# Kernel optimization log

Hardware: AMD Instinct MI355X
Metric: run time of the kernel (lower is better)

## Reference

```python
import jax, jax.numpy as jnp
import numpy as np

N = 100000      # nodes
E = 3200000     # edges
F_IN = 256      # in_channels
H = 64          # hidden_channels
C = 2           # out_channels
G = 128         # graphs in batch


def setup_inputs() -> dict:
    key = jax.random.key(0)
    ks = jax.random.split(key, 10)
    x = jax.random.normal(ks[0], (N, F_IN), jnp.float32)
    edge_index = jax.random.randint(ks[1], (2, E), 0, N, dtype=jnp.int64)
    batch = jnp.sort(jax.random.randint(ks[2], (N,), 0, G, dtype=jnp.int64))
    s = 0.05
    W1 = jax.random.normal(ks[3], (F_IN, H), jnp.float32) * s
    b1 = jnp.zeros((H,), jnp.float32)
    W2 = jax.random.normal(ks[4], (H, H), jnp.float32) * s
    b2 = jnp.zeros((H,), jnp.float32)
    fc_W = jax.random.normal(ks[5], (H, C), jnp.float32) * s
    fc_b = jnp.zeros((C,), jnp.float32)
    return {"x": x, "edge_index": edge_index, "batch": batch,
            "W1": W1, "b1": b1, "W2": W2, "b2": b2,
            "fc_W": fc_W, "fc_b": fc_b}


def _gcn_layer(h, src, dst, norm, W, b, n_nodes):
    # PyG GCNConv: linear transform first, then normalized aggregate, then bias
    h = h @ W                                   # [N, H]
    msg = h[src] * norm[:, None]                # [E+N, H] gather + scale
    out = jax.ops.segment_sum(msg, dst, num_segments=n_nodes)
    return out + b


def reference(x, edge_index, batch, W1, b1, W2, b2, fc_W, fc_b):
    n_nodes = x.shape[0]
    # add self loops (GCNConv default)
    loop = jnp.arange(n_nodes, dtype=edge_index.dtype)
    src = jnp.concatenate([edge_index[0], loop])
    dst = jnp.concatenate([edge_index[1], loop])
    # symmetric normalization D^{-1/2} (A+I) D^{-1/2}
    deg = jax.ops.segment_sum(jnp.ones_like(src, dtype=x.dtype), dst,
                              num_segments=n_nodes)
    deg_isqrt = jnp.where(deg > 0, jax.lax.rsqrt(deg), 0.0)
    norm = deg_isqrt[src] * deg_isqrt[dst]

    h = jax.nn.relu(_gcn_layer(x, src, dst, norm, W1, b1, n_nodes))
    h = jax.nn.relu(_gcn_layer(h, src, dst, norm, W2, b2, n_nodes))

    # global mean pool over graphs
    n_graphs = G
    sums = jax.ops.segment_sum(h, batch, num_segments=n_graphs)
    cnts = jax.ops.segment_sum(jnp.ones((n_nodes,), h.dtype), batch,
                               num_segments=n_graphs)
    pooled = sums / jnp.clip(cnts, 1.0)[:, None]  # [G, H]
    return pooled @ fc_W + fc_b                   # [G, C]
```

## Files before the change

### kernel.cpp

```cpp
#include <hip/hip_runtime.h>
#include <hip/hip_bf16.h>


#define F_IN 256
#define HDIM 64
#define BR_SHIFT 7
#define BRANGE 128
#define BCAP 4608
#define CHUNK 8192
#define NBK 788
#define HS_SCALE 32.0f

typedef short short8 __attribute__((ext_vector_type(8)));
typedef short short4v __attribute__((ext_vector_type(4)));
typedef float float4v __attribute__((ext_vector_type(4)));

__device__ __forceinline__ unsigned bf16_rn(float f) {
  unsigned u = __builtin_bit_cast(unsigned, f);
  return (u + 0x7FFFu + ((u >> 16) & 1u)) >> 16;
}
__device__ __forceinline__ float bf16_to_f32(unsigned h) {
  return __builtin_bit_cast(float, h << 16);
}
__device__ __forceinline__ unsigned char f32_to_fp8(float v) {
  unsigned r = (unsigned)__builtin_amdgcn_cvt_pk_fp8_f32(v, v, 0, false);
  return (unsigned char)(r & 0xFF);
}
__device__ __forceinline__ float4v fp8x4_to_f32x4(unsigned u) {
  float4v r;
  r[0] = __builtin_amdgcn_cvt_f32_fp8(u, 0);
  r[1] = __builtin_amdgcn_cvt_f32_fp8(u, 1);
  r[2] = __builtin_amdgcn_cvt_f32_fp8(u, 2);
  r[3] = __builtin_amdgcn_cvt_f32_fp8(u, 3);
  return r;
}

__global__ __launch_bounds__(256) void bin_kernel(
    const int* __restrict__ src, const int* __restrict__ dst,
    int* __restrict__ gcur, int* __restrict__ entries, int E, int nb) {
  __shared__ int out32[CHUNK];
  __shared__ int pref[NBK + 1];
  __shared__ int cur[NBK];
  __shared__ int gbase[NBK];
  __shared__ int sscan[256];
  const int tid = threadIdx.x;
  for (int i = tid; i < nb; i += 256) cur[i] = 0;
  __syncthreads();
  long e0 = (long)blockIdx.x * CHUNK;
  int cnt = (int)min((long)CHUNK, (long)E - e0);
  for (int i = tid; i < cnt; i += 256)
    atomicAdd(&cur[dst[e0 + i] >> BR_SHIFT], 1);
  __syncthreads();
  int b0 = tid * 4;
  int h[4];
  int s = 0;
#pragma unroll
  for (int i = 0; i < 4; ++i) {
    h[i] = (b0 + i < nb) ? cur[b0 + i] : 0;
    s += h[i];
  }
  int x = s;
  sscan[tid] = x;
  __syncthreads();
  for (int off = 1; off < 256; off <<= 1) {
    int t = (tid >= off) ? sscan[tid - off] : 0;
    __syncthreads();
    sscan[tid] += t;
    __syncthreads();
  }
  int run = sscan[tid] - x;
#pragma unroll
  for (int i = 0; i < 4; ++i) {
    if (b0 + i < nb) {
      pref[b0 + i] = run;
      cur[b0 + i] = run;
      if (h[i] > 0) gbase[b0 + i] = atomicAdd(&gcur[b0 + i], h[i]);
      run += h[i];
    }
  }
  if (tid == 0) pref[nb] = cnt;
  __syncthreads();
  for (int i = tid; i < cnt; i += 256) {
    int d = dst[e0 + i];
    int sv = src[e0 + i];
    int b = d >> BR_SHIFT;
    int r = atomicAdd(&cur[b], 1);
    out32[r] = ((d & (BRANGE - 1)) << 17) | sv;
  }
  __syncthreads();
  for (int j = tid; j < cnt; j += 256) {
    int lo = 0, hi = nb - 1;
    while (lo < hi) {
      int mid = (lo + hi + 1) >> 1;
      if (pref[mid] <= j) lo = mid; else hi = mid - 1;
    }
    int b = lo;
    int slot = gbase[b] + (j - pref[b]);
    if (slot < BCAP) entries[(size_t)b * BCAP + slot] = out32[j];
  }
}

__global__ __launch_bounds__(256) void bucket_scan_kernel(
    const int* __restrict__ gcur, int* __restrict__ bbase,
    int* __restrict__ rowptr, int nb, int N, int E) {
  __shared__ int sscan[256];
  const int tid = threadIdx.x;
  int b0 = tid * 4;
  int h[4];
  int s = 0;
#pragma unroll
  for (int i = 0; i < 4; ++i) {
    h[i] = (b0 + i < nb) ? min(gcur[b0 + i], BCAP) : 0;
    s += h[i];
  }
  int x = s;
  sscan[tid] = x;
  __syncthreads();
  for (int off = 1; off < 256; off <<= 1) {
    int t = (tid >= off) ? sscan[tid - off] : 0;
    __syncthreads();
    sscan[tid] += t;
    __syncthreads();
  }
  int run = sscan[tid] - x;
#pragma unroll
  for (int i = 0; i < 4; ++i) {
    if (b0 + i < nb) {
      bbase[b0 + i] = run;
      run += h[i];
    }
  }
  if (tid == 0) rowptr[N] = E;
}

__global__ __launch_bounds__(256) void csr_build_kernel(
    const int* __restrict__ entries, const int* __restrict__ gcur,
    const int* __restrict__ bbase, int* __restrict__ rowptr,
    float* __restrict__ dnorm, int* __restrict__ csr, int N) {
  __shared__ int lbuf[BCAP];
  __shared__ int lcnt[BRANGE];
  __shared__ int lpref[BRANGE];
  __shared__ int lcur[BRANGE];
  const int b = blockIdx.x, tid = threadIdx.x;
  const int v0 = b * BRANGE;
  const int nloc = min(BRANGE, N - v0);
  if (tid < BRANGE) lcnt[tid] = 0;
  __syncthreads();
  const int cnt = min(gcur[b], BCAP);
  const int base = bbase[b];
  const int* ep = entries + (size_t)b * BCAP;
  for (int i = tid; i < cnt; i += 256) atomicAdd(&lcnt[ep[i] >> 17], 1);
  __syncthreads();
  if (tid < BRANGE) lpref[tid] = lcnt[tid];
  __syncthreads();
  for (int off = 1; off < BRANGE; off <<= 1) {
    int t = 0;
    if (tid < BRANGE && tid >= off) t = lpref[tid - off];
    __syncthreads();
    if (tid < BRANGE) lpref[tid] += t;
    __syncthreads();
  }
  if (tid < BRANGE) {
    int excl = lpref[tid] - lcnt[tid];
    lcur[tid] = excl;
    if (tid < nloc) {
      rowptr[v0 + tid] = base + excl;
      dnorm[v0 + tid] = rsqrtf((float)lcnt[tid] + 1.0f);
    }
  }
  __syncthreads();
  for (int i = tid; i < cnt; i += 256) {
    int e = ep[i];
    int dl = e >> 17;
    int pos = atomicAdd(&lcur[dl], 1);
    if (pos < BCAP) lbuf[pos] = e & 0x1FFFF;
  }
  __syncthreads();
  int* outp = csr + base;
  for (int i = tid; i < cnt; i += 256) outp[i] = lbuf[i];
}

template <int K>
__global__ __launch_bounds__(256) void wfrag_kernel(
    const float* __restrict__ W, short* __restrict__ whi,
    short* __restrict__ wlo) {
  constexpr int KS = K / 32;
  int slot = blockIdx.x * 256 + threadIdx.x;
  if (slot >= 4 * KS * 64 * 8) return;
  int j = slot & 7;
  int lane = (slot >> 3) & 63;
  int fk = slot >> 9;
  int ks = fk % KS;
  int ct = fk / KS;
  int k = ks * 32 + (lane >> 4) * 8 + j;
  int n = ct * 16 + (lane & 15);
  float w = W[k * 64 + n];
  unsigned h = bf16_rn(w);
  unsigned l = bf16_rn(w - bf16_to_f32(h));
  whi[slot] = (short)h;
  wlo[slot] = (short)l;
}

template <int K>
__global__ __launch_bounds__(512) void mfma_gemm_kernel(
    const float* __restrict__ X, const short* __restrict__ whi,
    const short* __restrict__ wlo, const float* __restrict__ dnorm,
    unsigned char* __restrict__ out, int N) {
  constexpr int KS = K / 32;
  constexpr int P = K + 8;
  __shared__ __align__(16) short Ahi[64 * P];
  __shared__ __align__(16) short Alo[64 * P];
  const int tid = threadIdx.x;
  const long base = (long)blockIdx.x * 64;
  constexpr int C4 = K / 4;
  constexpr int NL = 64 * C4 / 512;
#pragma unroll
  for (int i = 0; i < NL; ++i) {
    int idx = tid + i * 512;
    int row = idx / C4;
    int c4 = idx % C4;
    long r = base + row;
    if (r >= N) r = N - 1;
    float4v v = *(const float4v*)&X[(size_t)r * K + c4 * 4];
    short4v hv, lv;
#pragma unroll
    for (int j = 0; j < 4; ++j) {
      float f = v[j];
      unsigned h = bf16_rn(f);
      unsigned l = bf16_rn(f - bf16_to_f32(h));
      hv[j] = (short)h;
      lv[j] = (short)l;
    }
    *(short4v*)&Ahi[row * P + c4 * 4] = hv;
    *(short4v*)&Alo[row * P + c4 * 4] = lv;
  }
  __syncthreads();
  const int lane = tid & 63;
  const int wave = tid >> 6;
  const int rt = wave & 3;
  const int chalf = wave >> 2;
  const int m = lane & 15;
  const int q = lane >> 4;
  const int arow = rt * 16 + m;
  float4v acc[2];
  acc[0] = (float4v){0.f, 0.f, 0.f, 0.f};
  acc[1] = (float4v){0.f, 0.f, 0.f, 0.f};
  for (int ks = 0; ks < KS; ++ks) {
    int koff = ks * 32 + q * 8;
    short8 ah = *(const short8*)&Ahi[arow * P + koff];
    short8 al = *(const short8*)&Alo[arow * P + koff];
#pragma unroll
    for (int cc = 0; cc < 2; ++cc) {
      int ct = chalf * 2 + cc;
      size_t fo = ((size_t)(ct * KS + ks) * 64 + lane) * 8;
      short8 bh = *(const short8*)&whi[fo];
      short8 bl = *(const short8*)&wlo[fo];
      acc[cc] = __builtin_amdgcn_mfma_f32_16x16x32_bf16(ah, bh, acc[cc], 0, 0, 0);
      acc[cc] = __builtin_amdgcn_mfma_f32_16x16x32_bf16(ah, bl, acc[cc], 0, 0, 0);
      acc[cc] = __builtin_amdgcn_mfma_f32_16x16x32_bf16(al, bh, acc[cc], 0, 0, 0);
    }
  }
#pragma unroll
  for (int reg = 0; reg < 4; ++reg) {
    long grow = base + rt * 16 + q * 4 + reg;
    if (grow < N) {
      float dn = dnorm[grow] * HS_SCALE;
#pragma unroll
      for (int cc = 0; cc < 2; ++cc) {
        int ct = chalf * 2 + cc;
        out[grow * 64 + ct * 16 + m] = f32_to_fp8(acc[cc][reg] * dn);
      }
    }
  }
}

__device__ __forceinline__ float4v gather_sum(
    const unsigned char* __restrict__ hs, const int* __restrict__ csr,
    int beg, int end, int v, int g, int q) {
  float4v a0 = {0.f, 0.f, 0.f, 0.f};
  float4v a1 = a0, a2 = a0, a3 = a0;
  const size_t co = (size_t)(q << 2);
  int j = beg;

#define GCN_SEL(u)                                                         \
    int t0 = csr[j + 4 * (u)], t1 = csr[j + 4 * (u) + 1],                  \
        t2 = csr[j + 4 * (u) + 2], t3 = csr[j + 4 * (u) + 3];              \
    int idx = g == 0 ? t0 : (g == 1 ? t1 : (g == 2 ? t2 : t3));

  for (; j + 32 <= end; j += 32) {
    unsigned u0, u1, u2, u3, u4, u5, u6, u7;
    { GCN_SEL(0) u0 = *(const unsigned*)(hs + (((size_t)idx) << 6) + co); }
    { GCN_SEL(1) u1 = *(const unsigned*)(hs + (((size_t)idx) << 6) + co); }
    { GCN_SEL(2) u2 = *(const unsigned*)(hs + (((size_t)idx) << 6) + co); }
    { GCN_SEL(3) u3 = *(const unsigned*)(hs + (((size_t)idx) << 6) + co); }
    { GCN_SEL(4) u4 = *(const unsigned*)(hs + (((size_t)idx) << 6) + co); }
    { GCN_SEL(5) u5 = *(const unsigned*)(hs + (((size_t)idx) << 6) + co); }
    { GCN_SEL(6) u6 = *(const unsigned*)(hs + (((size_t)idx) << 6) + co); }
    { GCN_SEL(7) u7 = *(const unsigned*)(hs + (((size_t)idx) << 6) + co); }
    a0 += fp8x4_to_f32x4(u0);
    a1 += fp8x4_to_f32x4(u1);
    a2 += fp8x4_to_f32x4(u2);
    a3 += fp8x4_to_f32x4(u3);
    a0 += fp8x4_to_f32x4(u4);
    a1 += fp8x4_to_f32x4(u5);
    a2 += fp8x4_to_f32x4(u6);
    a3 += fp8x4_to_f32x4(u7);
  }
  if (j < end) {
    const int r = end - j;
    unsigned u0, u1, u2, u3, u4, u5, u6, u7;
    float s0, s1, s2, s3, s4, s5, s6, s7;
#define GCN_MSEL(u, U, S)                                                  \
    { GCN_SEL(u)                                                           \
      bool p = (4 * (u) + g) < r;                                          \
      idx = p ? idx : v;                                                   \
      S = p ? 1.0f : 0.0f;                                                 \
      U = *(const unsigned*)(hs + (((size_t)idx) << 6) + co); }
    GCN_MSEL(0, u0, s0)
    GCN_MSEL(1, u1, s1)
    GCN_MSEL(2, u2, s2)
    GCN_MSEL(3, u3, s3)
    GCN_MSEL(4, u4, s4)
    GCN_MSEL(5, u5, s5)
    GCN_MSEL(6, u6, s6)
    GCN_MSEL(7, u7, s7)
    a0 += fp8x4_to_f32x4(u0) * s0;
    a1 += fp8x4_to_f32x4(u1) * s1;
    a2 += fp8x4_to_f32x4(u2) * s2;
    a3 += fp8x4_to_f32x4(u3) * s3;
    a0 += fp8x4_to_f32x4(u4) * s4;
    a1 += fp8x4_to_f32x4(u5) * s5;
    a2 += fp8x4_to_f32x4(u6) * s6;
    a3 += fp8x4_to_f32x4(u7) * s7;
#undef GCN_MSEL
  }
#undef GCN_SEL
  float4v t = (a0 + a1) + (a2 + a3);
#pragma unroll
  for (int k = 0; k < 4; ++k) {
    float x = t[k];
    x += __shfl_xor(x, 16);
    x += __shfl_xor(x, 32);
    t[k] = x;
  }
  return t;
}

__global__ __launch_bounds__(256) void gather_agg_kernel(
    const unsigned char* __restrict__ hs, const int* __restrict__ rowptr,
    const int* __restrict__ csr, const float* __restrict__ dnorm,
    const float* __restrict__ bias, float* __restrict__ hout, int N) {
  const int lane = threadIdx.x & 63;
  const int wave = __builtin_amdgcn_readfirstlane((int)(threadIdx.x >> 6));
  const int g = lane >> 4;
  const int q = lane & 15;
  int v = blockIdx.x * 4 + wave;
  if (v >= N) return;
  int beg = rowptr[v], end = rowptr[v + 1];
  float4v t = gather_sum(hs, csr, beg, end, v, g, q);
  unsigned su = *(const unsigned*)(hs + (((size_t)v) << 6) + (q << 2));
  float4v sf = fp8x4_to_f32x4(su);
  float dn = dnorm[v] * (1.0f / HS_SCALE);
  float4v b4 = *(const float4v*)&bias[q << 2];
  float4v o;
#pragma unroll
  for (int k = 0; k < 4; ++k)
    o[k] = fmaxf(dn * (t[k] + sf[k]) + b4[k], 0.f);
  if (g == 0) *(float4v*)&hout[((size_t)v << 6) + (q << 2)] = o;
}

__global__ __launch_bounds__(256) void gather_agg_pool_kernel(
    const unsigned char* __restrict__ hs, const int* __restrict__ rowptr,
    const int* __restrict__ csr, const float* __restrict__ dnorm,
    const float* __restrict__ bias, const int* __restrict__ batch,
    float* __restrict__ pooled, int N) {
  const int lane = threadIdx.x & 63;
  const int wave = __builtin_amdgcn_readfirstlane((int)(threadIdx.x >> 6));
  const int g = lane >> 4;
  const int q = lane & 15;
  int v = blockIdx.x * 4 + wave;
  if (v >= N) return;
  int beg = rowptr[v], end = rowptr[v + 1];
  float4v t = gather_sum(hs, csr, beg, end, v, g, q);
  unsigned su = *(const unsigned*)(hs + (((size_t)v) << 6) + (q << 2));
  float4v sf = fp8x4_to_f32x4(su);
  float dn = dnorm[v] * (1.0f / HS_SCALE);
  float4v b4 = *(const float4v*)&bias[q << 2];
  float4v o;
#pragma unroll
  for (int k = 0; k < 4; ++k)
    o[k] = fmaxf(dn * (t[k] + sf[k]) + b4[k], 0.f);
  int srcl = lane >> 2;
  float w0 = __shfl(o[0], srcl);
  float w1 = __shfl(o[1], srcl);
  float w2 = __shfl(o[2], srcl);
  float w3 = __shfl(o[3], srcl);
  int k = lane & 3;
  float val = k == 0 ? w0 : (k == 1 ? w1 : (k == 2 ? w2 : w3));
  int b = batch[v];
  atomicAdd(&pooled[((size_t)b << 6) + lane], val);
}

__global__ __launch_bounds__(256) void final_fc_kernel(
    const float* __restrict__ pooled, const int* __restrict__ batch,
    const float* __restrict__ fcW, const float* __restrict__ fcb,
    float* __restrict__ out, int G, int N) {
  int t = blockIdx.x * 256 + threadIdx.x;
  if (t < G * 2) {
    int g = t >> 1, c = t & 1;
    int lo = 0, hi = N;
    while (lo < hi) { int m = (lo + hi) >> 1; if (batch[m] < g) lo = m + 1; else hi = m; }
    int lb = lo;
    lo = 0; hi = N;
    while (lo < hi) { int m = (lo + hi) >> 1; if (batch[m] <= g) lo = m + 1; else hi = m; }
    int cntg = lo - lb;
    float inv = 1.0f / fmaxf((float)cntg, 1.0f);
    float acc = fcb[c];
#pragma unroll
    for (int h = 0; h < 64; ++h)
      acc = fmaf(pooled[g * 64 + h] * inv, fcW[h * 2 + c], acc);
    out[t] = acc;
  }
}

extern "C" void kernel_launch(void* const* d_in, const int* in_sizes, int n_in,
                              void* d_out, int out_size, void* d_ws, size_t ws_size,
                              hipStream_t stream) {
  const float* x   = (const float*)d_in[0];
  const int*   ei  = (const int*)d_in[1];
  const int*   bat = (const int*)d_in[2];
  const float* W1  = (const float*)d_in[3];
  const float* b1  = (const float*)d_in[4];
  const float* W2  = (const float*)d_in[5];
  const float* b2  = (const float*)d_in[6];
  const float* fcW = (const float*)d_in[7];
  const float* fcb = (const float*)d_in[8];
  float* out = (float*)d_out;

  const int N = in_sizes[0] / F_IN;
  const int E = in_sizes[1] / 2;
  const int G = out_size / 2;
  const int* src = ei;
  const int* dst = ei + E;
  const int nb  = (N + BRANGE - 1) >> BR_SHIFT;

  auto aln = [](size_t v) { return (v + 63) & ~(size_t)63; };
  char* w = (char*)d_ws;
  int*    entries = (int*)w;     w += aln((size_t)nb * BCAP * 4);
  int*    gcur    = (int*)w;     w += aln((size_t)nb * 4);
  int*    bbase   = (int*)w;     w += aln((size_t)nb * 4);
  int*    rowptr  = (int*)w;     w += aln((size_t)(N + 1) * 4);
  float*  dnorm   = (float*)w;   w += aln((size_t)N * 4);
  int*    csr     = (int*)w;     w += aln((size_t)(E + 64) * 4);
  unsigned char* hs = (unsigned char*)w; w += aln((size_t)N * 64);
  float*  h1      = (float*)w;   w += aln((size_t)N * 64 * 4);
  float*  pooled  = (float*)w;   w += aln((size_t)G * 64 * 4);
  short*  whi1    = (short*)w;   w += aln((size_t)F_IN * 64 * 2);
  short*  wlo1    = (short*)w;   w += aln((size_t)F_IN * 64 * 2);
  short*  whi2    = (short*)w;   w += aln((size_t)HDIM * 64 * 2);
  short*  wlo2    = (short*)w;   w += aln((size_t)HDIM * 64 * 2);

  hipMemsetAsync(gcur, 0, (size_t)nb * 4, stream);
  hipMemsetAsync(pooled, 0, (size_t)G * 64 * 4, stream);

  wfrag_kernel<F_IN><<<(F_IN * 64 * 8 / 8 + 255) / 256, 256, 0, stream>>>(W1, whi1, wlo1);
  wfrag_kernel<HDIM><<<(HDIM * 64 * 8 / 8 + 255) / 256, 256, 0, stream>>>(W2, whi2, wlo2);

  bin_kernel<<<(E + CHUNK - 1) / CHUNK, 256, 0, stream>>>(
      src, dst, gcur, entries, E, nb);
  bucket_scan_kernel<<<1, 256, 0, stream>>>(gcur, bbase, rowptr, nb, N, E);
  csr_build_kernel<<<nb, 256, 0, stream>>>(entries, gcur, bbase, rowptr,
                                           dnorm, csr, N);

  mfma_gemm_kernel<F_IN><<<(N + 63) / 64, 512, 0, stream>>>(
      x, whi1, wlo1, dnorm, hs, N);
  gather_agg_kernel<<<(N + 3) / 4, 256, 0, stream>>>(hs, rowptr, csr, dnorm, b1, h1, N);

  mfma_gemm_kernel<HDIM><<<(N + 63) / 64, 512, 0, stream>>>(
      h1, whi2, wlo2, dnorm, hs, N);
  gather_agg_pool_kernel<<<(N + 3) / 4, 256, 0, stream>>>(hs, rowptr, csr, dnorm, b2, bat, pooled, N);

  final_fc_kernel<<<1, 256, 0, stream>>>(pooled, bat, fcW, fcb, out, G, N);
}
```

Measured before the change: 496.8 us.

## Process two nodes per wave with interleaved gather volleys for memory-level parallelism

Each wave in both aggregation kernels now handles two consecutive nodes. The first two 32-edge volleys of both nodes are issued before any accumulation, so more independent gather loads are in flight at once, and the grid size is halved to match. With about 33 edges per node on average, most nodes need one or two volleys, so the interleaving covers the common case. In exchange, register pressure roughly doubles, which may lower occupancy, and every volley is now predicated, including full ones.

```diff
diff --git a/kernel.cpp b/kernel.cpp
--- a/kernel.cpp
+++ b/kernel.cpp
@@ -274,67 +274,53 @@
   }
 }
 
-__device__ __forceinline__ float4v gather_sum(
+struct VolReg {
+  unsigned u0, u1, u2, u3, u4, u5, u6, u7;
+  float s0, s1, s2, s3, s4, s5, s6, s7;
+};
+
+__device__ __forceinline__ VolReg volley_issue(
     const unsigned char* __restrict__ hs, const int* __restrict__ csr,
-    int beg, int end, int v, int g, int q) {
-  float4v a0 = {0.f, 0.f, 0.f, 0.f};
-  float4v a1 = a0, a2 = a0, a3 = a0;
-  const size_t co = (size_t)(q << 2);
-  int j = beg;
-
-#define GCN_SEL(u)                                                         \
+    int j, int end, int v, int g, size_t co) {
+  VolReg r;
+  const int rr = end - j;
+#define GCN_ISSUE(u, U, S)                                                 \
+  {                                                                        \
     int t0 = csr[j + 4 * (u)], t1 = csr[j + 4 * (u) + 1],                  \
         t2 = csr[j + 4 * (u) + 2], t3 = csr[j + 4 * (u) + 3];              \
-    int idx = g == 0 ? t0 : (g == 1 ? t1 : (g == 2 ? t2 : t3));
-
-  for (; j + 32 <= end; j += 32) {
-    unsigned u0, u1, u2, u3, u4, u5, u6, u7;
-    { GCN_SEL(0) u0 = *(const unsigned*)(hs + (((size_t)idx) << 6) + co); }
-    { GCN_SEL(1) u1 = *(const unsigned*)(hs + (((size_t)idx) << 6) + co); }
-    { GCN_SEL(2) u2 = *(const unsigned*)(hs + (((size_t)idx) << 6) + co); }
-    { GCN_SEL(3) u3 = *(const unsigned*)(hs + (((size_t)idx) << 6) + co); }
-    { GCN_SEL(4) u4 = *(const unsigned*)(hs + (((size_t)idx) << 6) + co); }
-    { GCN_SEL(5) u5 = *(const unsigned*)(hs + (((size_t)idx) << 6) + co); }
-    { GCN_SEL(6) u6 = *(const unsigned*)(hs + (((size_t)idx) << 6) + co); }
-    { GCN_SEL(7) u7 = *(const unsigned*)(hs + (((size_t)idx) << 6) + co); }
-    a0 += fp8x4_to_f32x4(u0);
-    a1 += fp8x4_to_f32x4(u1);
-    a2 += fp8x4_to_f32x4(u2);
-    a3 += fp8x4_to_f32x4(u3);
-    a0 += fp8x4_to_f32x4(u4);
-    a1 += fp8x4_to_f32x4(u5);
-    a2 += fp8x4_to_f32x4(u6);
-    a3 += fp8x4_to_f32x4(u7);
-  }
-  if (j < end) {
-    const int r = end - j;
-    unsigned u0, u1, u2, u3, u4, u5, u6, u7;
-    float s0, s1, s2, s3, s4, s5, s6, s7;
-#define GCN_MSEL(u, U, S)                                                  \
-    { GCN_SEL(u)                                                           \
-      bool p = (4 * (u) + g) < r;                                          \
-      idx = p ? idx : v;                                                   \
-      S = p ? 1.0f : 0.0f;                                                 \
-      U = *(const unsigned*)(hs + (((size_t)idx) << 6) + co); }
-    GCN_MSEL(0, u0, s0)
-    GCN_MSEL(1, u1, s1)
-    GCN_MSEL(2, u2, s2)
-    GCN_MSEL(3, u3, s3)
-    GCN_MSEL(4, u4, s4)
-    GCN_MSEL(5, u5, s5)
-    GCN_MSEL(6, u6, s6)
-    GCN_MSEL(7, u7, s7)
-    a0 += fp8x4_to_f32x4(u0) * s0;
-    a1 += fp8x4_to_f32x4(u1) * s1;
-    a2 += fp8x4_to_f32x4(u2) * s2;
-    a3 += fp8x4_to_f32x4(u3) * s3;
-    a0 += fp8x4_to_f32x4(u4) * s4;
-    a1 += fp8x4_to_f32x4(u5) * s5;
-    a2 += fp8x4_to_f32x4(u6) * s6;
-    a3 += fp8x4_to_f32x4(u7) * s7;
-#undef GCN_MSEL
-  }
-#undef GCN_SEL
+    int idx = g == 0 ? t0 : (g == 1 ? t1 : (g == 2 ? t2 : t3));            \
+    bool p = (4 * (u) + g) < rr;                                           \
+    idx = p ? idx : v;                                                     \
+    S = p ? 1.0f : 0.0f;                                                   \
+    U = *(const unsigned*)(hs + (((size_t)idx) << 6) + co);                \
+  }
+  GCN_ISSUE(0, r.u0, r.s0)
+  GCN_ISSUE(1, r.u1, r.s1)
+  GCN_ISSUE(2, r.u2, r.s2)
+  GCN_ISSUE(3, r.u3, r.s3)
+  GCN_ISSUE(4, r.u4, r.s4)
+  GCN_ISSUE(5, r.u5, r.s5)
+  GCN_ISSUE(6, r.u6, r.s6)
+  GCN_ISSUE(7, r.u7, r.s7)
+#undef GCN_ISSUE
+  return r;
+}
+
+__device__ __forceinline__ void volley_acc(const VolReg& r, float4v& a0,
+                                           float4v& a1, float4v& a2,
+                                           float4v& a3) {
+  a0 += fp8x4_to_f32x4(r.u0) * r.s0;
+  a1 += fp8x4_to_f32x4(r.u1) * r.s1;
+  a2 += fp8x4_to_f32x4(r.u2) * r.s2;
+  a3 += fp8x4_to_f32x4(r.u3) * r.s3;
+  a0 += fp8x4_to_f32x4(r.u4) * r.s4;
+  a1 += fp8x4_to_f32x4(r.u5) * r.s5;
+  a2 += fp8x4_to_f32x4(r.u6) * r.s6;
+  a3 += fp8x4_to_f32x4(r.u7) * r.s7;
+}
+
+__device__ __forceinline__ float4v fold4(float4v a0, float4v a1, float4v a2,
+                                         float4v a3) {
   float4v t = (a0 + a1) + (a2 + a3);
 #pragma unroll
   for (int k = 0; k < 4; ++k) {
@@ -344,6 +330,19 @@
     t[k] = x;
   }
   return t;
+}
+
+__device__ __forceinline__ float4v node_out(
+    const unsigned char* __restrict__ hs, const float* __restrict__ dnorm,
+    const float* __restrict__ bias, float4v t, int v, int q) {
+  unsigned su = *(const unsigned*)(hs + (((size_t)v) << 6) + (q << 2));
+  float4v sf = fp8x4_to_f32x4(su);
+  float dn = dnorm[v] * (1.0f / HS_SCALE);
+  float4v b4 = *(const float4v*)&bias[q << 2];
+  float4v o;
+#pragma unroll
+  for (int k = 0; k < 4; ++k) o[k] = fmaxf(dn * (t[k] + sf[k]) + b4[k], 0.f);
+  return o;
 }
 
 __global__ __launch_bounds__(256) void gather_agg_kernel(
@@ -354,19 +353,51 @@
   const int wave = __builtin_amdgcn_readfirstlane((int)(threadIdx.x >> 6));
   const int g = lane >> 4;
   const int q = lane & 15;
-  int v = blockIdx.x * 4 + wave;
-  if (v >= N) return;
-  int beg = rowptr[v], end = rowptr[v + 1];
-  float4v t = gather_sum(hs, csr, beg, end, v, g, q);
-  unsigned su = *(const unsigned*)(hs + (((size_t)v) << 6) + (q << 2));
-  float4v sf = fp8x4_to_f32x4(su);
-  float dn = dnorm[v] * (1.0f / HS_SCALE);
-  float4v b4 = *(const float4v*)&bias[q << 2];
-  float4v o;
-#pragma unroll
-  for (int k = 0; k < 4; ++k)
-    o[k] = fmaxf(dn * (t[k] + sf[k]) + b4[k], 0.f);
-  if (g == 0) *(float4v*)&hout[((size_t)v << 6) + (q << 2)] = o;
+  const size_t co = (size_t)(q << 2);
+  int v0 = blockIdx.x * 8 + wave * 2;
+  if (v0 >= N) return;
+  int v1 = v0 + 1;
+  bool hasB = v1 < N;
+  int beg0 = rowptr[v0];
+  int end0 = rowptr[v0 + 1];
+  int beg1 = end0;
+  int end1 = hasB ? rowptr[v1 + 1] : end0;
+
+  float4v z = {0.f, 0.f, 0.f, 0.f};
+  float4v aA0 = z, aA1 = z, aA2 = z, aA3 = z;
+  float4v aB0 = z, aB1 = z, aB2 = z, aB3 = z;
+
+  VolReg rA = volley_issue(hs, csr, beg0, end0, v0, g, co);
+  VolReg rB;
+  if (hasB) rB = volley_issue(hs, csr, beg1, end1, v1, g, co);
+  volley_acc(rA, aA0, aA1, aA2, aA3);
+  if (hasB) volley_acc(rB, aB0, aB1, aB2, aB3);
+
+  bool tA = beg0 + 32 < end0;
+  bool tB = hasB && (beg1 + 32 < end1);
+  if (tA || tB) {
+    VolReg r2A, r2B;
+    if (tA) r2A = volley_issue(hs, csr, beg0 + 32, end0, v0, g, co);
+    if (tB) r2B = volley_issue(hs, csr, beg1 + 32, end1, v1, g, co);
+    if (tA) volley_acc(r2A, aA0, aA1, aA2, aA3);
+    if (tB) volley_acc(r2B, aB0, aB1, aB2, aB3);
+  }
+  for (int j = beg0 + 64; j < end0; j += 32) {
+    VolReg r = volley_issue(hs, csr, j, end0, v0, g, co);
+    volley_acc(r, aA0, aA1, aA2, aA3);
+  }
+  if (hasB)
+    for (int j = beg1 + 64; j < end1; j += 32) {
+      VolReg r = volley_issue(hs, csr, j, end1, v1, g, co);
+      volley_acc(r, aB0, aB1, aB2, aB3);
+    }
+
+  float4v oA = node_out(hs, dnorm, bias, fold4(aA0, aA1, aA2, aA3), v0, q);
+  if (g == 0) *(float4v*)&hout[((size_t)v0 << 6) + (q << 2)] = oA;
+  if (hasB) {
+    float4v oB = node_out(hs, dnorm, bias, fold4(aB0, aB1, aB2, aB3), v1, q);
+    if (g == 0) *(float4v*)&hout[((size_t)v1 << 6) + (q << 2)] = oB;
+  }
 }
 
 __global__ __launch_bounds__(256) void gather_agg_pool_kernel(
@@ -378,27 +409,69 @@
   const int wave = __builtin_amdgcn_readfirstlane((int)(threadIdx.x >> 6));
   const int g = lane >> 4;
   const int q = lane & 15;
-  int v = blockIdx.x * 4 + wave;
-  if (v >= N) return;
-  int beg = rowptr[v], end = rowptr[v + 1];
-  float4v t = gather_sum(hs, csr, beg, end, v, g, q);
-  unsigned su = *(const unsigned*)(hs + (((size_t)v) << 6) + (q << 2));
-  float4v sf = fp8x4_to_f32x4(su);
-  float dn = dnorm[v] * (1.0f / HS_SCALE);
-  float4v b4 = *(const float4v*)&bias[q << 2];
-  float4v o;
-#pragma unroll
-  for (int k = 0; k < 4; ++k)
-    o[k] = fmaxf(dn * (t[k] + sf[k]) + b4[k], 0.f);
-  int srcl = lane >> 2;
-  float w0 = __shfl(o[0], srcl);
-  float w1 = __shfl(o[1], srcl);
-  float w2 = __shfl(o[2], srcl);
-  float w3 = __shfl(o[3], srcl);
-  int k = lane & 3;
-  float val = k == 0 ? w0 : (k == 1 ? w1 : (k == 2 ? w2 : w3));
-  int b = batch[v];
-  atomicAdd(&pooled[((size_t)b << 6) + lane], val);
+  const size_t co = (size_t)(q << 2);
+  int v0 = blockIdx.x * 8 + wave * 2;
+  if (v0 >= N) return;
+  int v1 = v0 + 1;
+  bool hasB = v1 < N;
+  int beg0 = rowptr[v0];
+  int end0 = rowptr[v0 + 1];
+  int beg1 = end0;
+  int end1 = hasB ? rowptr[v1 + 1] : end0;
+
+  float4v z = {0.f, 0.f, 0.f, 0.f};
+  float4v aA0 = z, aA1 = z, aA2 = z, aA3 = z;
+  float4v aB0 = z, aB1 = z, aB2 = z, aB3 = z;
+
+  VolReg rA = volley_issue(hs, csr, beg0, end0, v0, g, co);
+  VolReg rB;
+  if (hasB) rB = volley_issue(hs, csr, beg1, end1, v1, g, co);
+  volley_acc(rA, aA0, aA1, aA2, aA3);
+  if (hasB) volley_acc(rB, aB0, aB1, aB2, aB3);
+
+  bool tA = beg0 + 32 < end0;
+  bool tB = hasB && (beg1 + 32 < end1);
+  if (tA || tB) {
+    VolReg r2A, r2B;
+    if (tA) r2A = volley_issue(hs, csr, beg0 + 32, end0, v0, g, co);
+    if (tB) r2B = volley_issue(hs, csr, beg1 + 32, end1, v1, g, co);
+    if (tA) volley_acc(r2A, aA0, aA1, aA2, aA3);
+    if (tB) volley_acc(r2B, aB0, aB1, aB2, aB3);
+  }
+  for (int j = beg0 + 64; j < end0; j += 32) {
+    VolReg r = volley_issue(hs, csr, j, end0, v0, g, co);
+    volley_acc(r, aA0, aA1, aA2, aA3);
+  }
+  if (hasB)
+    for (int j = beg1 + 64; j < end1; j += 32) {
+      VolReg r = volley_issue(hs, csr, j, end1, v1, g, co);
+      volley_acc(r, aB0, aB1, aB2, aB3);
+    }
+
+  {
+    float4v o = node_out(hs, dnorm, bias, fold4(aA0, aA1, aA2, aA3), v0, q);
+    int srcl = lane >> 2;
+    float w0 = __shfl(o[0], srcl);
+    float w1 = __shfl(o[1], srcl);
+    float w2 = __shfl(o[2], srcl);
+    float w3 = __shfl(o[3], srcl);
+    int k = lane & 3;
+    float val = k == 0 ? w0 : (k == 1 ? w1 : (k == 2 ? w2 : w3));
+    int b = batch[v0];
+    atomicAdd(&pooled[((size_t)b << 6) + lane], val);
+  }
+  if (hasB) {
+    float4v o = node_out(hs, dnorm, bias, fold4(aB0, aB1, aB2, aB3), v1, q);
+    int srcl = lane >> 2;
+    float w0 = __shfl(o[0], srcl);
+    float w1 = __shfl(o[1], srcl);
+    float w2 = __shfl(o[2], srcl);
+    float w3 = __shfl(o[3], srcl);
+    int k = lane & 3;
+    float val = k == 0 ? w0 : (k == 1 ? w1 : (k == 2 ? w2 : w3));
+    int b = batch[v1];
+    atomicAdd(&pooled[((size_t)b << 6) + lane], val);
+  }
 }
 
 __global__ __launch_bounds__(256) void final_fc_kernel(
@@ -474,11 +547,11 @@
 
   mfma_gemm_kernel<F_IN><<<(N + 63) / 64, 512, 0, stream>>>(
       x, whi1, wlo1, dnorm, hs, N);
-  gather_agg_kernel<<<(N + 3) / 4, 256, 0, stream>>>(hs, rowptr, csr, dnorm, b1, h1, N);
+  gather_agg_kernel<<<(N + 7) / 8, 256, 0, stream>>>(hs, rowptr, csr, dnorm, b1, h1, N);
 
   mfma_gemm_kernel<HDIM><<<(N + 63) / 64, 512, 0, stream>>>(
       h1, whi2, wlo2, dnorm, hs, N);
-  gather_agg_pool_kernel<<<(N + 3) / 4, 256, 0, stream>>>(hs, rowptr, csr, dnorm, b2, bat, pooled, N);
+  gather_agg_pool_kernel<<<(N + 7) / 8, 256, 0, stream>>>(hs, rowptr, csr, dnorm, b2, bat, pooled, N);
 
   final_fc_kernel<<<1, 256, 0, stream>>>(pooled, bat, fcW, fcb, out, G, N);
 }
```

Result: no change. 504.4 us (+1.5%).
